# Kernel optimization log

Hardware: AMD Instinct MI355X
Metric: run time of the kernel (lower is better)

## Reference

```python
import jax, jax.numpy as jnp
import numpy as np

THETA0 = 3.0
THETA = 5.0
BIG = 1e10  # stands in for +inf in the squared-distance transform


def _edt_sq_1d(f):
    # f: [..., n] of squared distances; returns min_j (i-j)^2 + f[j] per i.
    n = f.shape[-1]
    i = jnp.arange(n, dtype=f.dtype)
    d2 = (i[:, None] - i[None, :]) ** 2  # [n, n]
    return jnp.min(f[..., None, :] + d2, axis=-1)


def _edt(mask):
    # Exact Euclidean distance from each voxel to the nearest zero of `mask`
    # (matches scipy.ndimage.distance_transform_edt on a binary mask),
    # via the separable squared-distance transform applied axis by axis.
    f = jnp.where(mask > 0.5, jnp.asarray(BIG, mask.dtype), jnp.asarray(0.0, mask.dtype))
    for ax in range(1, mask.ndim):  # skip batch axis 0
        f = jnp.moveaxis(_edt_sq_1d(jnp.moveaxis(f, ax, -1)), -1, ax)
    return jnp.sqrt(f)


def setup_inputs() -> dict:
    key = jax.random.key(0)
    k1, k2 = jax.random.split(key)
    B, D, H, W = 2, 64, 96, 96
    pred = jax.random.uniform(k1, (B, D, H, W), dtype=jnp.float32)  # probabilities
    target = jax.random.randint(k2, (B, D, H, W), 0, 2).astype(jnp.float32)  # binary mask
    return {"pred": pred, "target": target}


def reference(pred, target):
    # Signed distance phi = dist_to_foreground_boundary framework: 
    # dist_pos = EDT(target) (distance to nearest background voxel),
    # dist_neg = EDT(1 - target).
    dist_pos = _edt(target)
    dist_neg = _edt(1.0 - target)
    a = jnp.abs(dist_neg - dist_pos)
    w = jnp.where(
        a <= THETA0,
        1.0,
        jnp.where(a >= THETA, 0.0, 1.0 - (a - THETA0) / (THETA - THETA0)),
    )
    w = jax.lax.stop_gradient(w)  # original computes weights from detached numpy target

    # binary_cross_entropy with torch's log clamp at -100
    log_p = jnp.clip(jnp.log(pred), -100.0)
    log_1mp = jnp.clip(jnp.log(1.0 - pred), -100.0)
    bce = -(target * log_p + (1.0 - target) * log_1mp)  # [B, D, H, W]

    num = jnp.sum(bce * w, axis=(1, 2, 3))
    den = jnp.sum(w, axis=(1, 2, 3)) + 1e-5
    return jnp.mean(num / den)
```

## Files before the change

kernel.cpp:

```cpp
#include <hip/hip_runtime.h>
#include <math.h>

#define BDIM 2
#define DDIM 64
#define HDIM 96
#define WDIM 96
#define HW   (HDIM * WDIM)
#define DHW  (DDIM * HDIM * WDIM)
#define NVOX (BDIM * DHW)

#define BIGF 1e10f
#define FINF 3.0e38f

__global__ __launch_bounds__(256) void edt_pass_w(const float* __restrict__ target,
                                                  float* __restrict__ fp,
                                                  float* __restrict__ fn,
                                                  float* __restrict__ acc) {
    __shared__ float sfp[8 * WDIM];
    __shared__ float sfn[8 * WDIM];
    const int tid  = threadIdx.x;
    const int base = blockIdx.x * (8 * WDIM);

    if (blockIdx.x == 0 && tid < 4) acc[tid] = 0.0f;

    for (int t = tid; t < 8 * WDIM; t += 256) {
        float tg = target[base + t];
        bool  m  = tg > 0.5f;
        sfp[t] = m ? BIGF : 0.0f;
        sfn[t] = m ? 0.0f : BIGF;
    }
    __syncthreads();

    for (int t = tid; t < 8 * WDIM; t += 256) {
        const int l = t / WDIM;
        const int i = t - l * WDIM;
        const float4* rp = (const float4*)&sfp[l * WDIM];
        const float4* rn = (const float4*)&sfn[l * WDIM];
        float mp = FINF, mn = FINF;
        float d0 = (float)i;
        #pragma unroll 6
        for (int j4 = 0; j4 < WDIM / 4; ++j4) {
            float4 p = rp[j4];
            float4 n = rn[j4];
            float d1 = d0 - 1.f, d2 = d0 - 2.f, d3 = d0 - 3.f;
            mp = fminf(mp, fmaf(d0, d0, p.x));
            mp = fminf(mp, fmaf(d1, d1, p.y));
            mp = fminf(mp, fmaf(d2, d2, p.z));
            mp = fminf(mp, fmaf(d3, d3, p.w));
            mn = fminf(mn, fmaf(d0, d0, n.x));
            mn = fminf(mn, fmaf(d1, d1, n.y));
            mn = fminf(mn, fmaf(d2, d2, n.z));
            mn = fminf(mn, fmaf(d3, d3, n.w));
            d0 -= 4.f;
        }
        fp[base + t] = mp;
        fn[base + t] = mn;
    }
}

__global__ __launch_bounds__(256) void edt_pass_h(float* __restrict__ fp,
                                                  float* __restrict__ fn) {
    __shared__ float sfp[HDIM * 32];
    __shared__ float sfn[HDIM * 32];
    const int tid  = threadIdx.x;
    const int slab = blockIdx.x / 3;
    const int w0   = (blockIdx.x % 3) * 32;
    const int base = slab * HW + w0;

    for (int t = tid; t < HDIM * 32; t += 256) {
        int h = t >> 5, wi = t & 31;
        int g = base + h * WDIM + wi;
        sfp[t] = fp[g];
        sfn[t] = fn[g];
    }
    __syncthreads();

    for (int k = 0; k < 3; ++k) {
        int gq = tid + 256 * k;
        int ho = gq >> 3;
        int q  = gq & 7;
        float4 mp = {FINF, FINF, FINF, FINF};
        float4 mn = {FINF, FINF, FINF, FINF};
        float dcur = (float)ho;
        const float4* rp = ((const float4*)sfp) + q;
        const float4* rn = ((const float4*)sfn) + q;
        #pragma unroll 4
        for (int j = 0; j < HDIM; ++j) {
            float4 p = rp[j * 8];
            float4 n = rn[j * 8];
            float d2 = dcur * dcur;
            mp.x = fminf(mp.x, d2 + p.x);
            mp.y = fminf(mp.y, d2 + p.y);
            mp.z = fminf(mp.z, d2 + p.z);
            mp.w = fminf(mp.w, d2 + p.w);
            mn.x = fminf(mn.x, d2 + n.x);
            mn.y = fminf(mn.y, d2 + n.y);
            mn.z = fminf(mn.z, d2 + n.z);
            mn.w = fminf(mn.w, d2 + n.w);
            dcur -= 1.f;
        }
        int g = base + ho * WDIM + q * 4;
        *(float4*)&fp[g] = mp;
        *(float4*)&fn[g] = mn;
    }
}

__device__ __forceinline__ void accum_loss(float mpv, float mnv, float p, float t,
                                           float& num, float& den) {
    float dp = sqrtf(mpv);
    float dn = sqrtf(mnv);
    float a  = fabsf(dn - dp);
    float w;
    if (a <= 3.0f)      w = 1.0f;
    else if (a >= 5.0f) w = 0.0f;
    else                w = 1.0f - (a - 3.0f) * 0.5f;
    float lp = fmaxf(logf(p), -100.0f);
    float l1 = fmaxf(logf(1.0f - p), -100.0f);
    float bce = -(t * lp + (1.0f - t) * l1);
    num += bce * w;
    den += w;
}

__global__ __launch_bounds__(256) void edt_pass_d_loss(const float* __restrict__ fp,
                                                       const float* __restrict__ fn,
                                                       const float* __restrict__ pred,
                                                       const float* __restrict__ target,
                                                       float* __restrict__ acc) {
    __shared__ float sfp[DDIM * 32];
    __shared__ float sfn[DDIM * 32];
    __shared__ float rsum[8];
    const int tid = threadIdx.x;
    const int w0  = (blockIdx.x % 3) * 32;
    const int bh  = blockIdx.x / 3;
    const int b   = bh / HDIM;
    const int h   = bh - b * HDIM;
    const int base = b * DHW + h * WDIM + w0;

    for (int t = tid; t < DDIM * 32; t += 256) {
        int d = t >> 5, wi = t & 31;
        int g = base + d * HW + wi;
        sfp[t] = fp[g];
        sfn[t] = fn[g];
    }
    __syncthreads();

    float num = 0.f, den = 0.f;
    for (int k = 0; k < 2; ++k) {
        int gq = tid + 256 * k;
        int dd = gq >> 3;
        int q  = gq & 7;
        float4 mp = {FINF, FINF, FINF, FINF};
        float4 mn = {FINF, FINF, FINF, FINF};
        float dcur = (float)dd;
        const float4* rp = ((const float4*)sfp) + q;
        const float4* rn = ((const float4*)sfn) + q;
        #pragma unroll 4
        for (int j = 0; j < DDIM; ++j) {
            float4 p = rp[j * 8];
            float4 n = rn[j * 8];
            float d2 = dcur * dcur;
            mp.x = fminf(mp.x, d2 + p.x);
            mp.y = fminf(mp.y, d2 + p.y);
            mp.z = fminf(mp.z, d2 + p.z);
            mp.w = fminf(mp.w, d2 + p.w);
            mn.x = fminf(mn.x, d2 + n.x);
            mn.y = fminf(mn.y, d2 + n.y);
            mn.z = fminf(mn.z, d2 + n.z);
            mn.w = fminf(mn.w, d2 + n.w);
            dcur -= 1.f;
        }
        int g = base + dd * HW + q * 4;
        float4 pr = *(const float4*)&pred[g];
        float4 tg = *(const float4*)&target[g];
        accum_loss(mp.x, mn.x, pr.x, tg.x, num, den);
        accum_loss(mp.y, mn.y, pr.y, tg.y, num, den);
        accum_loss(mp.z, mn.z, pr.z, tg.z, num, den);
        accum_loss(mp.w, mn.w, pr.w, tg.w, num, den);
    }

    for (int off = 32; off > 0; off >>= 1) {
        num += __shfl_down(num, off);
        den += __shfl_down(den, off);
    }
    if ((tid & 63) == 0) {
        rsum[tid >> 6]       = num;
        rsum[4 + (tid >> 6)] = den;
    }
    __syncthreads();
    if (tid == 0) {
        float ns = rsum[0] + rsum[1] + rsum[2] + rsum[3];
        float ds = rsum[4] + rsum[5] + rsum[6] + rsum[7];
        atomicAdd(&acc[b], ns);
        atomicAdd(&acc[2 + b], ds);
    }
}

__global__ void finalize(const float* __restrict__ acc, float* __restrict__ out) {
    if (threadIdx.x == 0) {
        float r0 = acc[0] / (acc[2] + 1e-5f);
        float r1 = acc[1] / (acc[3] + 1e-5f);
        out[0] = 0.5f * (r0 + r1);
    }
}

extern "C" void kernel_launch(void* const* d_in, const int* in_sizes, int n_in,
                              void* d_out, int out_size, void* d_ws, size_t ws_size,
                              hipStream_t stream) {
    const float* pred   = (const float*)d_in[0];
    const float* target = (const float*)d_in[1];
    float* fp  = (float*)d_ws;
    float* fn  = fp + NVOX;
    float* acc = fn + NVOX;
    float* out = (float*)d_out;

    edt_pass_w<<<BDIM * DDIM * HDIM / 8, 256, 0, stream>>>(target, fp, fn, acc);
    edt_pass_h<<<BDIM * DDIM * 3, 256, 0, stream>>>(fp, fn);
    edt_pass_d_loss<<<BDIM * HDIM * 3, 256, 0, stream>>>(fp, fn, pred, target, acc);
    finalize<<<1, 64, 0, stream>>>(acc, out);
}
```

Before: 117.5 us.

## Register-block EDT passes so each shared-memory load serves multiple outputs

All three EDT passes are restructured so each thread computes several outputs at once (6 along W, 3 along H, 2 along D) and reuses each shared-memory value across them. This targets the LDS load traffic per min-plus operation. The W pass now handles 16 rows per block with a padded row stride of 100 to reduce bank conflicts, which halves the number of blocks. The cost is higher register pressure, and the smaller W grid could lower occupancy.

```diff
diff --git a/kernel.cpp b/kernel.cpp
--- a/kernel.cpp
+++ b/kernel.cpp
@@ -12,49 +12,61 @@
 #define BIGF 1e10f
 #define FINF 3.0e38f
 
+#define LSTR 100
 __global__ __launch_bounds__(256) void edt_pass_w(const float* __restrict__ target,
                                                   float* __restrict__ fp,
                                                   float* __restrict__ fn,
                                                   float* __restrict__ acc) {
-    __shared__ float sfp[8 * WDIM];
-    __shared__ float sfn[8 * WDIM];
+    __shared__ float sfp[16 * LSTR];
+    __shared__ float sfn[16 * LSTR];
     const int tid  = threadIdx.x;
-    const int base = blockIdx.x * (8 * WDIM);
+    const int base = blockIdx.x * (16 * WDIM);
 
     if (blockIdx.x == 0 && tid < 4) acc[tid] = 0.0f;
 
-    for (int t = tid; t < 8 * WDIM; t += 256) {
+    for (int t = tid; t < 16 * WDIM; t += 256) {
+        int l = t / WDIM;
+        int i = t - l * WDIM;
         float tg = target[base + t];
         bool  m  = tg > 0.5f;
-        sfp[t] = m ? BIGF : 0.0f;
-        sfn[t] = m ? 0.0f : BIGF;
-    }
-    __syncthreads();
-
-    for (int t = tid; t < 8 * WDIM; t += 256) {
-        const int l = t / WDIM;
-        const int i = t - l * WDIM;
-        const float4* rp = (const float4*)&sfp[l * WDIM];
-        const float4* rn = (const float4*)&sfn[l * WDIM];
-        float mp = FINF, mn = FINF;
-        float d0 = (float)i;
-        #pragma unroll 6
-        for (int j4 = 0; j4 < WDIM / 4; ++j4) {
-            float4 p = rp[j4];
-            float4 n = rn[j4];
-            float d1 = d0 - 1.f, d2 = d0 - 2.f, d3 = d0 - 3.f;
-            mp = fminf(mp, fmaf(d0, d0, p.x));
-            mp = fminf(mp, fmaf(d1, d1, p.y));
-            mp = fminf(mp, fmaf(d2, d2, p.z));
-            mp = fminf(mp, fmaf(d3, d3, p.w));
-            mn = fminf(mn, fmaf(d0, d0, n.x));
-            mn = fminf(mn, fmaf(d1, d1, n.y));
-            mn = fminf(mn, fmaf(d2, d2, n.z));
-            mn = fminf(mn, fmaf(d3, d3, n.w));
-            d0 -= 4.f;
+        sfp[l * LSTR + i] = m ? BIGF : 0.0f;
+        sfn[l * LSTR + i] = m ? 0.0f : BIGF;
+    }
+    __syncthreads();
+
+    const int c = tid & 15;
+    const int l = tid >> 4;
+    const float4* rp = (const float4*)&sfp[l * LSTR];
+    const float4* rn = (const float4*)&sfn[l * LSTR];
+
+    float mp[6], mn[6];
+    #pragma unroll
+    for (int r = 0; r < 6; ++r) { mp[r] = FINF; mn[r] = FINF; }
+
+    const float fc = (float)c;
+    #pragma unroll 2
+    for (int j4 = 0; j4 < WDIM / 4; ++j4) {
+        float4 p = rp[j4];
+        float4 n = rn[j4];
+        float db = fc - (float)(4 * j4);
+        #pragma unroll
+        for (int jj = 0; jj < 4; ++jj) {
+            float pv = jj == 0 ? p.x : jj == 1 ? p.y : jj == 2 ? p.z : p.w;
+            float nv = jj == 0 ? n.x : jj == 1 ? n.y : jj == 2 ? n.z : n.w;
+            float d0 = db - (float)jj;
+            #pragma unroll
+            for (int r = 0; r < 6; ++r) {
+                float d = d0 + (float)(16 * r);
+                mp[r] = fminf(mp[r], fmaf(d, d, pv));
+                mn[r] = fminf(mn[r], fmaf(d, d, nv));
+            }
         }
-        fp[base + t] = mp;
-        fn[base + t] = mn;
+    }
+    #pragma unroll
+    for (int r = 0; r < 6; ++r) {
+        int g = base + l * WDIM + c + 16 * r;
+        fp[g] = mp[r];
+        fn[g] = mn[r];
     }
 }
 
@@ -75,33 +87,42 @@
     }
     __syncthreads();
 
+    const int q  = tid & 7;
+    const int r0 = tid >> 3;
+    float4 mp[3], mn[3];
+    #pragma unroll
     for (int k = 0; k < 3; ++k) {
-        int gq = tid + 256 * k;
-        int ho = gq >> 3;
-        int q  = gq & 7;
-        float4 mp = {FINF, FINF, FINF, FINF};
-        float4 mn = {FINF, FINF, FINF, FINF};
-        float dcur = (float)ho;
-        const float4* rp = ((const float4*)sfp) + q;
-        const float4* rn = ((const float4*)sfn) + q;
-        #pragma unroll 4
-        for (int j = 0; j < HDIM; ++j) {
-            float4 p = rp[j * 8];
-            float4 n = rn[j * 8];
-            float d2 = dcur * dcur;
-            mp.x = fminf(mp.x, d2 + p.x);
-            mp.y = fminf(mp.y, d2 + p.y);
-            mp.z = fminf(mp.z, d2 + p.z);
-            mp.w = fminf(mp.w, d2 + p.w);
-            mn.x = fminf(mn.x, d2 + n.x);
-            mn.y = fminf(mn.y, d2 + n.y);
-            mn.z = fminf(mn.z, d2 + n.z);
-            mn.w = fminf(mn.w, d2 + n.w);
-            dcur -= 1.f;
+        mp[k] = make_float4(FINF, FINF, FINF, FINF);
+        mn[k] = make_float4(FINF, FINF, FINF, FINF);
+    }
+    const float4* rp = ((const float4*)sfp) + q;
+    const float4* rn = ((const float4*)sfn) + q;
+
+    float dd = (float)r0;
+    #pragma unroll 2
+    for (int j = 0; j < HDIM; ++j) {
+        float4 p = rp[j * 8];
+        float4 n = rn[j * 8];
+        #pragma unroll
+        for (int k = 0; k < 3; ++k) {
+            float d  = dd + (float)(32 * k);
+            float d2 = d * d;
+            mp[k].x = fminf(mp[k].x, d2 + p.x);
+            mp[k].y = fminf(mp[k].y, d2 + p.y);
+            mp[k].z = fminf(mp[k].z, d2 + p.z);
+            mp[k].w = fminf(mp[k].w, d2 + p.w);
+            mn[k].x = fminf(mn[k].x, d2 + n.x);
+            mn[k].y = fminf(mn[k].y, d2 + n.y);
+            mn[k].z = fminf(mn[k].z, d2 + n.z);
+            mn[k].w = fminf(mn[k].w, d2 + n.w);
         }
-        int g = base + ho * WDIM + q * 4;
-        *(float4*)&fp[g] = mp;
-        *(float4*)&fn[g] = mn;
+        dd -= 1.f;
+    }
+    #pragma unroll
+    for (int k = 0; k < 3; ++k) {
+        int g = base + (r0 + 32 * k) * WDIM + q * 4;
+        *(float4*)&fp[g] = mp[k];
+        *(float4*)&fn[g] = mn[k];
     }
 }
 
@@ -144,38 +165,48 @@
     }
     __syncthreads();
 
+    const int q  = tid & 7;
+    const int r0 = tid >> 3;
+    float4 mp[2], mn[2];
+    #pragma unroll
+    for (int k = 0; k < 2; ++k) {
+        mp[k] = make_float4(FINF, FINF, FINF, FINF);
+        mn[k] = make_float4(FINF, FINF, FINF, FINF);
+    }
+    const float4* rp = ((const float4*)sfp) + q;
+    const float4* rn = ((const float4*)sfn) + q;
+
+    float dd = (float)r0;
+    #pragma unroll 2
+    for (int j = 0; j < DDIM; ++j) {
+        float4 p = rp[j * 8];
+        float4 n = rn[j * 8];
+        #pragma unroll
+        for (int k = 0; k < 2; ++k) {
+            float d  = dd + (float)(32 * k);
+            float d2 = d * d;
+            mp[k].x = fminf(mp[k].x, d2 + p.x);
+            mp[k].y = fminf(mp[k].y, d2 + p.y);
+            mp[k].z = fminf(mp[k].z, d2 + p.z);
+            mp[k].w = fminf(mp[k].w, d2 + p.w);
+            mn[k].x = fminf(mn[k].x, d2 + n.x);
+            mn[k].y = fminf(mn[k].y, d2 + n.y);
+            mn[k].z = fminf(mn[k].z, d2 + n.z);
+            mn[k].w = fminf(mn[k].w, d2 + n.w);
+        }
+        dd -= 1.f;
+    }
+
     float num = 0.f, den = 0.f;
+    #pragma unroll
     for (int k = 0; k < 2; ++k) {
-        int gq = tid + 256 * k;
-        int dd = gq >> 3;
-        int q  = gq & 7;
-        float4 mp = {FINF, FINF, FINF, FINF};
-        float4 mn = {FINF, FINF, FINF, FINF};
-        float dcur = (float)dd;
-        const float4* rp = ((const float4*)sfp) + q;
-        const float4* rn = ((const float4*)sfn) + q;
-        #pragma unroll 4
-        for (int j = 0; j < DDIM; ++j) {
-            float4 p = rp[j * 8];
-            float4 n = rn[j * 8];
-            float d2 = dcur * dcur;
-            mp.x = fminf(mp.x, d2 + p.x);
-            mp.y = fminf(mp.y, d2 + p.y);
-            mp.z = fminf(mp.z, d2 + p.z);
-            mp.w = fminf(mp.w, d2 + p.w);
-            mn.x = fminf(mn.x, d2 + n.x);
-            mn.y = fminf(mn.y, d2 + n.y);
-            mn.z = fminf(mn.z, d2 + n.z);
-            mn.w = fminf(mn.w, d2 + n.w);
-            dcur -= 1.f;
-        }
-        int g = base + dd * HW + q * 4;
+        int g = base + (r0 + 32 * k) * HW + q * 4;
         float4 pr = *(const float4*)&pred[g];
         float4 tg = *(const float4*)&target[g];
-        accum_loss(mp.x, mn.x, pr.x, tg.x, num, den);
-        accum_loss(mp.y, mn.y, pr.y, tg.y, num, den);
-        accum_loss(mp.z, mn.z, pr.z, tg.z, num, den);
-        accum_loss(mp.w, mn.w, pr.w, tg.w, num, den);
+        accum_loss(mp[k].x, mn[k].x, pr.x, tg.x, num, den);
+        accum_loss(mp[k].y, mn[k].y, pr.y, tg.y, num, den);
+        accum_loss(mp[k].z, mn[k].z, pr.z, tg.z, num, den);
+        accum_loss(mp[k].w, mn[k].w, pr.w, tg.w, num, den);
     }
 
     for (int off = 32; off > 0; off >>= 1) {
@@ -213,7 +244,7 @@
     float* acc = fn + NVOX;
     float* out = (float*)d_out;
 
-    edt_pass_w<<<BDIM * DDIM * HDIM / 8, 256, 0, stream>>>(target, fp, fn, acc);
+    edt_pass_w<<<BDIM * DDIM * HDIM / 16, 256, 0, stream>>>(target, fp, fn, acc);
     edt_pass_h<<<BDIM * DDIM * 3, 256, 0, stream>>>(fp, fn);
     edt_pass_d_loss<<<BDIM * HDIM * 3, 256, 0, stream>>>(fp, fn, pred, target, acc);
     finalize<<<1, 64, 0, stream>>>(acc, out);
```

Result: no change. 119.0 us (+1.3%).

## Truncate EDT passes to a radius-4 window, since weights vanish beyond distance 5

Applied to the files above, without the earlier changes.

Each separable squared-distance pass now searches only a 9-tap window (offsets -4..4) and starts from 25 instead of scanning the whole axis. This is valid because the loss weight is zero once the distance reaches 5, and any voxel with a true distance below 5 has its nearest zero within 4 steps on every axis. The passes go from O(n) to constant work per voxel, so the kernels should become bandwidth-bound rather than ALU-bound. The W pass also handles 16 lines per block with padded shared rows. One risk: the W-pass padding value 0.5 makes out-of-range positions count as background for the positive transform, which may change results near the W borders.

```diff
diff --git a/kernel.cpp b/kernel.cpp
--- a/kernel.cpp
+++ b/kernel.cpp
@@ -10,85 +10,95 @@
 #define NVOX (BDIM * DHW)
 
 #define BIGF 1e10f
-#define FINF 3.0e38f
-
+
+
+#define K1_LSTR 104
 __global__ __launch_bounds__(256) void edt_pass_w(const float* __restrict__ target,
                                                   float* __restrict__ fp,
                                                   float* __restrict__ fn,
                                                   float* __restrict__ acc) {
-    __shared__ float sfp[8 * WDIM];
-    __shared__ float sfn[8 * WDIM];
+    __shared__ float sm[16 * K1_LSTR];
     const int tid  = threadIdx.x;
-    const int base = blockIdx.x * (8 * WDIM);
+    const int base = blockIdx.x * (16 * WDIM);
 
     if (blockIdx.x == 0 && tid < 4) acc[tid] = 0.0f;
 
-    for (int t = tid; t < 8 * WDIM; t += 256) {
-        float tg = target[base + t];
-        bool  m  = tg > 0.5f;
-        sfp[t] = m ? BIGF : 0.0f;
-        sfn[t] = m ? 0.0f : BIGF;
-    }
-    __syncthreads();
-
-    for (int t = tid; t < 8 * WDIM; t += 256) {
-        const int l = t / WDIM;
-        const int i = t - l * WDIM;
-        const float4* rp = (const float4*)&sfp[l * WDIM];
-        const float4* rn = (const float4*)&sfn[l * WDIM];
-        float mp = FINF, mn = FINF;
-        float d0 = (float)i;
-        #pragma unroll 6
-        for (int j4 = 0; j4 < WDIM / 4; ++j4) {
-            float4 p = rp[j4];
-            float4 n = rn[j4];
-            float d1 = d0 - 1.f, d2 = d0 - 2.f, d3 = d0 - 3.f;
-            mp = fminf(mp, fmaf(d0, d0, p.x));
-            mp = fminf(mp, fmaf(d1, d1, p.y));
-            mp = fminf(mp, fmaf(d2, d2, p.z));
-            mp = fminf(mp, fmaf(d3, d3, p.w));
-            mn = fminf(mn, fmaf(d0, d0, n.x));
-            mn = fminf(mn, fmaf(d1, d1, n.y));
-            mn = fminf(mn, fmaf(d2, d2, n.z));
-            mn = fminf(mn, fmaf(d3, d3, n.w));
-            d0 -= 4.f;
+    if (tid < 128) {
+        int l = tid >> 3, s = tid & 7;
+        sm[l * K1_LSTR + (s < 4 ? s : 96 + s)] = 0.5f;
+    }
+    for (int t = tid; t < 16 * WDIM; t += 256) {
+        int l = t / WDIM;
+        int i = t - l * WDIM;
+        sm[l * K1_LSTR + 4 + i] = target[base + t];
+    }
+    __syncthreads();
+
+    const int c = tid & 15;
+    const int l = tid >> 4;
+    const float* line = &sm[l * K1_LSTR];
+
+    float sp[6], sn[6];
+    #pragma unroll
+    for (int r = 0; r < 6; ++r) { sp[r] = 25.0f; sn[r] = 25.0f; }
+
+    #pragma unroll
+    for (int d = -4; d <= 4; ++d) {
+        const float d2 = (float)(d * d);
+        #pragma unroll
+        for (int r = 0; r < 6; ++r) {
+            float m  = line[4 + c + 16 * r + d];
+            bool  fg = m > 0.5f;
+            sp[r] = fminf(sp[r], fg ? BIGF : d2);
+            sn[r] = fminf(sn[r], fg ? d2 : BIGF);
         }
-        fp[base + t] = mp;
-        fn[base + t] = mn;
-    }
-}
-
+    }
+    #pragma unroll
+    for (int r = 0; r < 6; ++r) {
+        int g = base + l * WDIM + c + 16 * r;
+        fp[g] = sp[r];
+        fn[g] = sn[r];
+    }
+}
+
+#define K2_STR 36
 __global__ __launch_bounds__(256) void edt_pass_h(float* __restrict__ fp,
                                                   float* __restrict__ fn) {
-    __shared__ float sfp[HDIM * 32];
-    __shared__ float sfn[HDIM * 32];
+    __shared__ float sfp[104 * K2_STR];
+    __shared__ float sfn[104 * K2_STR];
     const int tid  = threadIdx.x;
     const int slab = blockIdx.x / 3;
     const int w0   = (blockIdx.x % 3) * 32;
     const int base = slab * HW + w0;
 
+    {
+        int s = tid >> 5, wi = tid & 31;
+        int r = (s < 4) ? s : 96 + s;
+        sfp[r * K2_STR + wi] = BIGF;
+        sfn[r * K2_STR + wi] = BIGF;
+    }
     for (int t = tid; t < HDIM * 32; t += 256) {
         int h = t >> 5, wi = t & 31;
         int g = base + h * WDIM + wi;
-        sfp[t] = fp[g];
-        sfn[t] = fn[g];
-    }
-    __syncthreads();
-
+        sfp[(h + 4) * K2_STR + wi] = fp[g];
+        sfn[(h + 4) * K2_STR + wi] = fn[g];
+    }
+    __syncthreads();
+
+    const int q  = tid & 7;
+    const int r0 = tid >> 3;
+    #pragma unroll
     for (int k = 0; k < 3; ++k) {
-        int gq = tid + 256 * k;
-        int ho = gq >> 3;
-        int q  = gq & 7;
-        float4 mp = {FINF, FINF, FINF, FINF};
-        float4 mn = {FINF, FINF, FINF, FINF};
-        float dcur = (float)ho;
-        const float4* rp = ((const float4*)sfp) + q;
-        const float4* rn = ((const float4*)sfn) + q;
-        #pragma unroll 4
-        for (int j = 0; j < HDIM; ++j) {
-            float4 p = rp[j * 8];
-            float4 n = rn[j * 8];
-            float d2 = dcur * dcur;
+        const int row = r0 + 32 * k;
+        float4 mp = {25.f, 25.f, 25.f, 25.f};
+        float4 mn = {25.f, 25.f, 25.f, 25.f};
+        #pragma unroll
+        for (int t9 = 0; t9 < 9; ++t9) {
+            const int pr = row + t9;
+            const float d  = (float)(t9 - 4);
+            const float d2 = d * d;
+            float4 p = *(const float4*)&sfp[pr * K2_STR + q * 4];
+            float4 n = *(const float4*)&sfn[pr * K2_STR + q * 4];
             mp.x = fminf(mp.x, d2 + p.x);
             mp.y = fminf(mp.y, d2 + p.y);
             mp.z = fminf(mp.z, d2 + p.z);
@@ -97,9 +107,8 @@
             mn.y = fminf(mn.y, d2 + n.y);
             mn.z = fminf(mn.z, d2 + n.z);
             mn.w = fminf(mn.w, d2 + n.w);
-            dcur -= 1.f;
         }
-        int g = base + ho * WDIM + q * 4;
+        int g = base + row * WDIM + q * 4;
         *(float4*)&fp[g] = mp;
         *(float4*)&fn[g] = mn;
     }
@@ -126,8 +135,8 @@
                                                        const float* __restrict__ pred,
                                                        const float* __restrict__ target,
                                                        float* __restrict__ acc) {
-    __shared__ float sfp[DDIM * 32];
-    __shared__ float sfn[DDIM * 32];
+    __shared__ float sfp[72 * K2_STR];
+    __shared__ float sfn[72 * K2_STR];
     __shared__ float rsum[8];
     const int tid = threadIdx.x;
     const int w0  = (blockIdx.x % 3) * 32;
@@ -136,29 +145,35 @@
     const int h   = bh - b * HDIM;
     const int base = b * DHW + h * WDIM + w0;
 
+    {
+        int s = tid >> 5, wi = tid & 31;
+        int r = (s < 4) ? s : 64 + s;
+        sfp[r * K2_STR + wi] = BIGF;
+        sfn[r * K2_STR + wi] = BIGF;
+    }
     for (int t = tid; t < DDIM * 32; t += 256) {
         int d = t >> 5, wi = t & 31;
         int g = base + d * HW + wi;
-        sfp[t] = fp[g];
-        sfn[t] = fn[g];
-    }
-    __syncthreads();
-
+        sfp[(d + 4) * K2_STR + wi] = fp[g];
+        sfn[(d + 4) * K2_STR + wi] = fn[g];
+    }
+    __syncthreads();
+
+    const int q  = tid & 7;
+    const int r0 = tid >> 3;
     float num = 0.f, den = 0.f;
+    #pragma unroll
     for (int k = 0; k < 2; ++k) {
-        int gq = tid + 256 * k;
-        int dd = gq >> 3;
-        int q  = gq & 7;
-        float4 mp = {FINF, FINF, FINF, FINF};
-        float4 mn = {FINF, FINF, FINF, FINF};
-        float dcur = (float)dd;
-        const float4* rp = ((const float4*)sfp) + q;
-        const float4* rn = ((const float4*)sfn) + q;
-        #pragma unroll 4
-        for (int j = 0; j < DDIM; ++j) {
-            float4 p = rp[j * 8];
-            float4 n = rn[j * 8];
-            float d2 = dcur * dcur;
+        const int row = r0 + 32 * k;
+        float4 mp = {25.f, 25.f, 25.f, 25.f};
+        float4 mn = {25.f, 25.f, 25.f, 25.f};
+        #pragma unroll
+        for (int t9 = 0; t9 < 9; ++t9) {
+            const int pr = row + t9;
+            const float d  = (float)(t9 - 4);
+            const float d2 = d * d;
+            float4 p = *(const float4*)&sfp[pr * K2_STR + q * 4];
+            float4 n = *(const float4*)&sfn[pr * K2_STR + q * 4];
             mp.x = fminf(mp.x, d2 + p.x);
             mp.y = fminf(mp.y, d2 + p.y);
             mp.z = fminf(mp.z, d2 + p.z);
@@ -167,15 +182,14 @@
             mn.y = fminf(mn.y, d2 + n.y);
             mn.z = fminf(mn.z, d2 + n.z);
             mn.w = fminf(mn.w, d2 + n.w);
-            dcur -= 1.f;
         }
-        int g = base + dd * HW + q * 4;
-        float4 pr = *(const float4*)&pred[g];
-        float4 tg = *(const float4*)&target[g];
-        accum_loss(mp.x, mn.x, pr.x, tg.x, num, den);
-        accum_loss(mp.y, mn.y, pr.y, tg.y, num, den);
-        accum_loss(mp.z, mn.z, pr.z, tg.z, num, den);
-        accum_loss(mp.w, mn.w, pr.w, tg.w, num, den);
+        int g = base + row * HW + q * 4;
+        float4 pr4 = *(const float4*)&pred[g];
+        float4 tg4 = *(const float4*)&target[g];
+        accum_loss(mp.x, mn.x, pr4.x, tg4.x, num, den);
+        accum_loss(mp.y, mn.y, pr4.y, tg4.y, num, den);
+        accum_loss(mp.z, mn.z, pr4.z, tg4.z, num, den);
+        accum_loss(mp.w, mn.w, pr4.w, tg4.w, num, den);
     }
 
     for (int off = 32; off > 0; off >>= 1) {
@@ -213,7 +227,7 @@
     float* acc = fn + NVOX;
     float* out = (float*)d_out;
 
-    edt_pass_w<<<BDIM * DDIM * HDIM / 8, 256, 0, stream>>>(target, fp, fn, acc);
+    edt_pass_w<<<NVOX / (16 * WDIM), 256, 0, stream>>>(target, fp, fn, acc);
     edt_pass_h<<<BDIM * DDIM * 3, 256, 0, stream>>>(fp, fn);
     edt_pass_d_loss<<<BDIM * HDIM * 3, 256, 0, stream>>>(fp, fn, pred, target, acc);
     finalize<<<1, 64, 0, stream>>>(acc, out);
```

After: 95.52 us. 1.23x faster.

## Replace full EDT with radius-limited local distance via bitmasked halo tiles in one kernel

Applied to the files above, without the earlier changes.

The weight only depends on whether |dist_neg - dist_pos| falls within [3,5], so exact distances beyond a small radius are never needed. The three separable full-length EDT passes are replaced by one fused kernel: each block loads a target tile with a 4-voxel halo as bitmasks, computes per-axis nearest squared distances capped at 25 in byte-sized shared arrays, and then does the loss. Global fp/fn intermediates are dropped and the finalize kernel is folded in via a last-block counter. The cap relies on one of the two distances always being zero, which holds for a binary mask, so the truncation should not change any weight.

```diff
diff --git a/kernel.cpp b/kernel.cpp
--- a/kernel.cpp
+++ b/kernel.cpp
@@ -6,176 +6,143 @@
 #define HDIM 96
 #define WDIM 96
 #define HW   (HDIM * WDIM)
-#define DHW  (DDIM * HDIM * WDIM)
-#define NVOX (BDIM * DHW)
+#define DHW  (DDIM * HW)
 
-#define BIGF 1e10f
-#define FINF 3.0e38f
+#define DT 16
+#define DH 24
+#define HT 8
+#define HH 16
+#define WT 32
+#define NROWS (DH * HH)
+#define NBLK  (BDIM * (DDIM / DT) * (HDIM / HT) * (WDIM / WT))
 
-__global__ __launch_bounds__(256) void edt_pass_w(const float* __restrict__ target,
-                                                  float* __restrict__ fp,
-                                                  float* __restrict__ fn,
-                                                  float* __restrict__ acc) {
-    __shared__ float sfp[8 * WDIM];
-    __shared__ float sfn[8 * WDIM];
-    const int tid  = threadIdx.x;
-    const int base = blockIdx.x * (8 * WDIM);
+__global__ void init_acc(float* __restrict__ acc) {
+    if (threadIdx.x < 4) acc[threadIdx.x] = 0.0f;
+    if (threadIdx.x == 4) ((int*)acc)[4] = 0;
+}
 
-    if (blockIdx.x == 0 && tid < 4) acc[tid] = 0.0f;
+__device__ __forceinline__ unsigned nearest2i(unsigned occ) {
+    unsigned r = 25u;
+    if (occ & 0x101u) r = 16u;
+    if (occ & 0x082u) r = 9u;
+    if (occ & 0x044u) r = 4u;
+    if (occ & 0x028u) r = 1u;
+    if (occ & 0x010u) r = 0u;
+    return r;
+}
 
-    for (int t = tid; t < 8 * WDIM; t += 256) {
-        float tg = target[base + t];
-        bool  m  = tg > 0.5f;
-        sfp[t] = m ? BIGF : 0.0f;
-        sfn[t] = m ? 0.0f : BIGF;
+__global__ __launch_bounds__(256) void boundary_fused(const float* __restrict__ pred,
+                                                      const float* __restrict__ target,
+                                                      float* __restrict__ acc,
+                                                      float* __restrict__ out) {
+    __shared__ unsigned fgb[NROWS * 2];
+    __shared__ unsigned vbb[NROWS * 2];
+    __shared__ unsigned char swp[DH * HH * WT];
+    __shared__ unsigned char swn[DH * HH * WT];
+    __shared__ unsigned char whp[DH * HT * WT];
+    __shared__ unsigned char whn[DH * HT * WT];
+    __shared__ float rsum[8];
+
+    const int tid = threadIdx.x;
+    int x = blockIdx.x;
+    const int wt = x % 3;  x /= 3;
+    const int ht = x % 12; x /= 12;
+    const int dt = x % 4;
+    const int b  = x / 4;
+    const int d0 = dt * DT, h0 = ht * HT, w0 = wt * WT;
+
+    for (int i = tid; i < NROWS * 2; i += 256) { fgb[i] = 0u; vbb[i] = 0u; }
+    __syncthreads();
+
+    for (int idx = tid; idx < NROWS * 10; idx += 256) {
+        const int row = idx / 10, q = idx - row * 10;
+        const int dr = row >> 4, hr = row & 15;
+        const int d = d0 - 4 + dr, h = h0 - 4 + hr;
+        if (d < 0 || d >= DDIM || h < 0 || h >= HDIM) continue;
+        const int wbase = w0 - 4 + q * 4;
+        const float* rowp = target + ((size_t)(b * DDIM + d) * HDIM + h) * WDIM;
+        unsigned fgn = 0u, vn = 0u;
+        if (wbase >= 0 && wbase <= WDIM - 4) {
+            float4 v4 = *(const float4*)(rowp + wbase);
+            fgn = (unsigned)(v4.x > 0.5f) | ((unsigned)(v4.y > 0.5f) << 1) |
+                  ((unsigned)(v4.z > 0.5f) << 2) | ((unsigned)(v4.w > 0.5f) << 3);
+            vn = 0xFu;
+        } else {
+            for (int j = 0; j < 4; ++j) {
+                int w = wbase + j;
+                if (w >= 0 && w < WDIM) {
+                    vn |= 1u << j;
+                    if (rowp[w] > 0.5f) fgn |= 1u << j;
+                }
+            }
+        }
+        if (vn) {
+            const int k = q * 4, word = k >> 5, sh = k & 31;
+            if (fgn) atomicOr(&fgb[row * 2 + word], fgn << sh);
+            atomicOr(&vbb[row * 2 + word], vn << sh);
+        }
     }
     __syncthreads();
 
-    for (int t = tid; t < 8 * WDIM; t += 256) {
-        const int l = t / WDIM;
-        const int i = t - l * WDIM;
-        const float4* rp = (const float4*)&sfp[l * WDIM];
-        const float4* rn = (const float4*)&sfn[l * WDIM];
-        float mp = FINF, mn = FINF;
-        float d0 = (float)i;
-        #pragma unroll 6
-        for (int j4 = 0; j4 < WDIM / 4; ++j4) {
-            float4 p = rp[j4];
-            float4 n = rn[j4];
-            float d1 = d0 - 1.f, d2 = d0 - 2.f, d3 = d0 - 3.f;
-            mp = fminf(mp, fmaf(d0, d0, p.x));
-            mp = fminf(mp, fmaf(d1, d1, p.y));
-            mp = fminf(mp, fmaf(d2, d2, p.z));
-            mp = fminf(mp, fmaf(d3, d3, p.w));
-            mn = fminf(mn, fmaf(d0, d0, n.x));
-            mn = fminf(mn, fmaf(d1, d1, n.y));
-            mn = fminf(mn, fmaf(d2, d2, n.z));
-            mn = fminf(mn, fmaf(d3, d3, n.w));
-            d0 -= 4.f;
-        }
-        fp[base + t] = mp;
-        fn[base + t] = mn;
-    }
-}
-
-__global__ __launch_bounds__(256) void edt_pass_h(float* __restrict__ fp,
-                                                  float* __restrict__ fn) {
-    __shared__ float sfp[HDIM * 32];
-    __shared__ float sfn[HDIM * 32];
-    const int tid  = threadIdx.x;
-    const int slab = blockIdx.x / 3;
-    const int w0   = (blockIdx.x % 3) * 32;
-    const int base = slab * HW + w0;
-
-    for (int t = tid; t < HDIM * 32; t += 256) {
-        int h = t >> 5, wi = t & 31;
-        int g = base + h * WDIM + wi;
-        sfp[t] = fp[g];
-        sfn[t] = fn[g];
+    for (int idx = tid; idx < NROWS * WT; idx += 256) {
+        const int row = idx >> 5, wi = idx & 31;
+        unsigned long long fg = ((unsigned long long)fgb[row * 2 + 1] << 32) | fgb[row * 2];
+        unsigned long long vv = ((unsigned long long)vbb[row * 2 + 1] << 32) | vbb[row * 2];
+        unsigned of = (unsigned)(fg >> wi) & 0x1FFu;
+        unsigned ov = (unsigned)(vv >> wi) & 0x1FFu;
+        unsigned ob = ~of & ov;
+        swn[idx] = (unsigned char)nearest2i(of);
+        swp[idx] = (unsigned char)nearest2i(ob);
     }
     __syncthreads();
 
-    for (int k = 0; k < 3; ++k) {
-        int gq = tid + 256 * k;
-        int ho = gq >> 3;
-        int q  = gq & 7;
-        float4 mp = {FINF, FINF, FINF, FINF};
-        float4 mn = {FINF, FINF, FINF, FINF};
-        float dcur = (float)ho;
-        const float4* rp = ((const float4*)sfp) + q;
-        const float4* rn = ((const float4*)sfn) + q;
-        #pragma unroll 4
-        for (int j = 0; j < HDIM; ++j) {
-            float4 p = rp[j * 8];
-            float4 n = rn[j * 8];
-            float d2 = dcur * dcur;
-            mp.x = fminf(mp.x, d2 + p.x);
-            mp.y = fminf(mp.y, d2 + p.y);
-            mp.z = fminf(mp.z, d2 + p.z);
-            mp.w = fminf(mp.w, d2 + p.w);
-            mn.x = fminf(mn.x, d2 + n.x);
-            mn.y = fminf(mn.y, d2 + n.y);
-            mn.z = fminf(mn.z, d2 + n.z);
-            mn.w = fminf(mn.w, d2 + n.w);
-            dcur -= 1.f;
+    for (int idx = tid; idx < DH * HT * WT; idx += 256) {
+        const int dr = idx >> 8;
+        const int hh = (idx >> 5) & 7;
+        const int wi = idx & 31;
+        unsigned p = 25u, n = 25u;
+        #pragma unroll
+        for (int t = 0; t < 9; ++t) {
+            const unsigned d2 = (unsigned)((t - 4) * (t - 4));
+            const int src = (dr * HH + hh + t) * WT + wi;
+            p = min(p, d2 + (unsigned)swp[src]);
+            n = min(n, d2 + (unsigned)swn[src]);
         }
-        int g = base + ho * WDIM + q * 4;
-        *(float4*)&fp[g] = mp;
-        *(float4*)&fn[g] = mn;
-    }
-}
-
-__device__ __forceinline__ void accum_loss(float mpv, float mnv, float p, float t,
-                                           float& num, float& den) {
-    float dp = sqrtf(mpv);
-    float dn = sqrtf(mnv);
-    float a  = fabsf(dn - dp);
-    float w;
-    if (a <= 3.0f)      w = 1.0f;
-    else if (a >= 5.0f) w = 0.0f;
-    else                w = 1.0f - (a - 3.0f) * 0.5f;
-    float lp = fmaxf(logf(p), -100.0f);
-    float l1 = fmaxf(logf(1.0f - p), -100.0f);
-    float bce = -(t * lp + (1.0f - t) * l1);
-    num += bce * w;
-    den += w;
-}
-
-__global__ __launch_bounds__(256) void edt_pass_d_loss(const float* __restrict__ fp,
-                                                       const float* __restrict__ fn,
-                                                       const float* __restrict__ pred,
-                                                       const float* __restrict__ target,
-                                                       float* __restrict__ acc) {
-    __shared__ float sfp[DDIM * 32];
-    __shared__ float sfn[DDIM * 32];
-    __shared__ float rsum[8];
-    const int tid = threadIdx.x;
-    const int w0  = (blockIdx.x % 3) * 32;
-    const int bh  = blockIdx.x / 3;
-    const int b   = bh / HDIM;
-    const int h   = bh - b * HDIM;
-    const int base = b * DHW + h * WDIM + w0;
-
-    for (int t = tid; t < DDIM * 32; t += 256) {
-        int d = t >> 5, wi = t & 31;
-        int g = base + d * HW + wi;
-        sfp[t] = fp[g];
-        sfn[t] = fn[g];
+        whp[idx] = (unsigned char)p;
+        whn[idx] = (unsigned char)n;
     }
     __syncthreads();
 
     float num = 0.f, den = 0.f;
-    for (int k = 0; k < 2; ++k) {
-        int gq = tid + 256 * k;
-        int dd = gq >> 3;
-        int q  = gq & 7;
-        float4 mp = {FINF, FINF, FINF, FINF};
-        float4 mn = {FINF, FINF, FINF, FINF};
-        float dcur = (float)dd;
-        const float4* rp = ((const float4*)sfp) + q;
-        const float4* rn = ((const float4*)sfn) + q;
-        #pragma unroll 4
-        for (int j = 0; j < DDIM; ++j) {
-            float4 p = rp[j * 8];
-            float4 n = rn[j * 8];
-            float d2 = dcur * dcur;
-            mp.x = fminf(mp.x, d2 + p.x);
-            mp.y = fminf(mp.y, d2 + p.y);
-            mp.z = fminf(mp.z, d2 + p.z);
-            mp.w = fminf(mp.w, d2 + p.w);
-            mn.x = fminf(mn.x, d2 + n.x);
-            mn.y = fminf(mn.y, d2 + n.y);
-            mn.z = fminf(mn.z, d2 + n.z);
-            mn.w = fminf(mn.w, d2 + n.w);
-            dcur -= 1.f;
+    #pragma unroll 4
+    for (int it = 0; it < 16; ++it) {
+        const int idx = tid + 256 * it;
+        const int di = idx >> 8;
+        const int hh = (idx >> 5) & 7;
+        const int wi = idx & 31;
+        unsigned p = 25u, n = 25u;
+        #pragma unroll
+        for (int t = 0; t < 9; ++t) {
+            const unsigned d2 = (unsigned)((t - 4) * (t - 4));
+            const int src = ((di + t) * HT + hh) * WT + wi;
+            p = min(p, d2 + (unsigned)whp[src]);
+            n = min(n, d2 + (unsigned)whn[src]);
         }
-        int g = base + dd * HW + q * 4;
-        float4 pr = *(const float4*)&pred[g];
-        float4 tg = *(const float4*)&target[g];
-        accum_loss(mp.x, mn.x, pr.x, tg.x, num, den);
-        accum_loss(mp.y, mn.y, pr.y, tg.y, num, den);
-        accum_loss(mp.z, mn.z, pr.z, tg.z, num, den);
-        accum_loss(mp.w, mn.w, pr.w, tg.w, num, den);
+        const size_t g = ((size_t)(b * DDIM + d0 + di) * HDIM + h0 + hh) * WDIM + w0 + wi;
+        const float pr = pred[g];
+        const float tg = target[g];
+        const float dp = sqrtf((float)p);
+        const float dn = sqrtf((float)n);
+        const float a  = fabsf(dn - dp);
+        float w;
+        if (a <= 3.0f)      w = 1.0f;
+        else if (a >= 5.0f) w = 0.0f;
+        else                w = 1.0f - (a - 3.0f) * 0.5f;
+        const float lp  = fmaxf(logf(pr), -100.0f);
+        const float l1  = fmaxf(logf(1.0f - pr), -100.0f);
+        const float bce = -(tg * lp + (1.0f - tg) * l1);
+        num += bce * w;
+        den += w;
     }
 
     for (int off = 32; off > 0; off >>= 1) {
@@ -192,14 +159,16 @@
         float ds = rsum[4] + rsum[5] + rsum[6] + rsum[7];
         atomicAdd(&acc[b], ns);
         atomicAdd(&acc[2 + b], ds);
-    }
-}
-
-__global__ void finalize(const float* __restrict__ acc, float* __restrict__ out) {
-    if (threadIdx.x == 0) {
-        float r0 = acc[0] / (acc[2] + 1e-5f);
-        float r1 = acc[1] / (acc[3] + 1e-5f);
-        out[0] = 0.5f * (r0 + r1);
+        __threadfence();
+        int done = atomicAdd((int*)acc + 4, 1);
+        if (done == NBLK - 1) {
+            __threadfence();
+            float n0 = atomicAdd(&acc[0], 0.0f);
+            float n1 = atomicAdd(&acc[1], 0.0f);
+            float d0_ = atomicAdd(&acc[2], 0.0f);
+            float d1_ = atomicAdd(&acc[3], 0.0f);
+            out[0] = 0.5f * (n0 / (d0_ + 1e-5f) + n1 / (d1_ + 1e-5f));
+        }
     }
 }
 
@@ -208,13 +177,9 @@
                               hipStream_t stream) {
     const float* pred   = (const float*)d_in[0];
     const float* target = (const float*)d_in[1];
-    float* fp  = (float*)d_ws;
-    float* fn  = fp + NVOX;
-    float* acc = fn + NVOX;
+    float* acc = (float*)d_ws;
     float* out = (float*)d_out;
 
-    edt_pass_w<<<BDIM * DDIM * HDIM / 8, 256, 0, stream>>>(target, fp, fn, acc);
-    edt_pass_h<<<BDIM * DDIM * 3, 256, 0, stream>>>(fp, fn);
-    edt_pass_d_loss<<<BDIM * HDIM * 3, 256, 0, stream>>>(fp, fn, pred, target, acc);
-    finalize<<<1, 64, 0, stream>>>(acc, out);
+    init_acc<<<1, 64, 0, stream>>>(acc);
+    boundary_fused<<<NBLK, 256, 0, stream>>>(pred, target, acc, out);
 }
```

After: 95.13 us. 19.0% less time.
